# Kernel optimization log

Measured on AMD Instinct MI355X. Metric: run time of the kernel, lower is better.

Reference implementation:

```python
import jax, jax.numpy as jnp
import numpy as np
from jax import lax

SR = 4096.0        # sample_rate_Hz
N_LAYERS = 4
N_STATE = 64       # state_dim
E = 2              # d_inner (expand=2, d_model=1)
K = 4              # depthwise conv kernel
DT_RANK = 1
B, L = 32, 4096


def setup_inputs() -> dict:
    key = jax.random.key(0)
    ks = jax.random.split(key, 10)
    s = 0.02
    x = jax.random.normal(ks[0], (B, L), dtype=jnp.float32)
    W_in   = jax.random.normal(ks[1], (N_LAYERS, 1, 2 * E), jnp.float32) * 1.0
    conv_w = jax.random.normal(ks[2], (N_LAYERS, E, K), jnp.float32) * 0.5
    conv_b = jnp.zeros((N_LAYERS, E), jnp.float32)
    W_x    = jax.random.normal(ks[3], (N_LAYERS, E, DT_RANK + 2 * N_STATE), jnp.float32) * s
    W_dt   = jax.random.normal(ks[4], (N_LAYERS, DT_RANK, E), jnp.float32) * s
    b_dt   = jnp.zeros((N_LAYERS, E), jnp.float32)
    # S4D-real style init: A = -exp(A_log), A_log = log(1..N)
    A_log  = jnp.broadcast_to(jnp.log(jnp.arange(1, N_STATE + 1, dtype=jnp.float32)), (N_LAYERS, E, N_STATE)).copy()
    D_skip = jnp.ones((N_LAYERS, E), jnp.float32)
    W_out  = jax.random.normal(ks[5], (N_LAYERS, E, 1), jnp.float32) * s
    return {"x": x, "W_in": W_in, "conv_w": conv_w, "conv_b": conv_b, "W_x": W_x,
            "W_dt": W_dt, "b_dt": b_dt, "A_log": A_log, "D_skip": D_skip, "W_out": W_out}


def _causal_dwconv(u, w, b):
    # u: [B,L,E], w: [E,K] depthwise causal conv
    Klen = w.shape[1]
    up = jnp.pad(u, ((0, 0), (Klen - 1, 0), (0, 0)))
    y = sum(up[:, k:k + u.shape[1], :] * w[None, None, :, k] for k in range(Klen))
    return y + b


def _selective_scan(u, delta, A, Bm, Cm, Dv):
    # u,delta: [B,L,E]; A: [E,N]; Bm,Cm: [B,L,N]; Dv: [E]
    dA = jnp.exp(delta[..., None] * A)                       # [B,L,E,N]
    dBu = delta[..., None] * Bm[:, :, None, :] * u[..., None]  # [B,L,E,N]

    def step(h, inp):
        dA_t, dBu_t, C_t = inp                               # [B,E,N],[B,E,N],[B,N]
        h = dA_t * h + dBu_t
        y = jnp.einsum('ben,bn->be', h, C_t)
        return h, y

    h0 = jnp.zeros((u.shape[0],) + A.shape, dtype=u.dtype)
    _, ys = lax.scan(step, h0, (dA.transpose(1, 0, 2, 3), dBu.transpose(1, 0, 2, 3), Cm.transpose(1, 0, 2)))
    return ys.transpose(1, 0, 2) + u * Dv                    # [B,L,E]


def _mamba_block(x, W_in, conv_w, conv_b, W_x, W_dt, b_dt, A_log, D_skip, W_out):
    # x: [B,L,1]
    xz = x @ W_in                                            # [B,L,2E]
    u, z = xz[..., :E], xz[..., E:]
    u = jax.nn.silu(_causal_dwconv(u, conv_w, conv_b))       # [B,L,E]
    proj = u @ W_x                                           # [B,L,DT_RANK+2N]
    dt = proj[..., :DT_RANK]
    Bm = proj[..., DT_RANK:DT_RANK + N_STATE]
    Cm = proj[..., DT_RANK + N_STATE:]
    delta = jax.nn.softplus(dt @ W_dt + b_dt) / SR           # [B,L,E], timestep tied to sample rate
    A = -jnp.exp(A_log)                                      # [E,N]
    y = _selective_scan(u, delta, A, Bm, Cm, D_skip)
    y = y * jax.nn.silu(z)
    return y @ W_out + x                                     # residual, [B,L,1]


def reference(x, W_in, conv_w, conv_b, W_x, W_dt, b_dt, A_log, D_skip, W_out):
    h = x[..., None]                                         # [B,L,1]
    for i in range(N_LAYERS):
        h = _mamba_block(h, W_in[i], conv_w[i], conv_b[i], W_x[i], W_dt[i],
                         b_dt[i], A_log[i], D_skip[i], W_out[i])
    return h[..., 0]
```

## Files before the change

kernel.cpp:

```cpp
#include <hip/hip_runtime.h>
#include <hip/hip_bf16.h>


constexpr int   Bsz = 32;
constexpr int   Lsz = 4096;
constexpr int   NC  = 32;
constexpr int   CL  = 128;
constexpr float SRinv = 1.0f / 4096.0f;

__device__ __forceinline__ float sigmoidf_(float v) {
    return 1.0f / (1.0f + __expf(-v));
}

__global__ __launch_bounds__(128) void k_chunk_scan(
    const float* __restrict__ xin,
    const float* __restrict__ W_in,
    const float* __restrict__ conv_w,
    const float* __restrict__ conv_b,
    const float* __restrict__ W_x,
    const float* __restrict__ W_dt,
    const float* __restrict__ b_dt,
    const float* __restrict__ A_log,
    float4* __restrict__ ud,
    float*  __restrict__ Pc,
    float*  __restrict__ Sc)
{
    const int c = blockIdx.x, b = blockIdx.y, tid = threadIdx.x;
    __shared__ float  xs[CL + 3];
    __shared__ float4 s_ud[CL];
    const int base = b * Lsz + c * CL;

    for (int i = tid; i < CL + 3; i += 128) {
        int l = c * CL + i - 3;
        xs[i] = (l >= 0) ? xin[b * Lsz + l] : 0.0f;
    }
    __syncthreads();

    {
        const int t = tid;
        float x0 = xs[t], x1 = xs[t + 1], x2 = xs[t + 2], x3 = xs[t + 3];
        float u[2];
        #pragma unroll
        for (int e = 0; e < 2; e++) {
            float v = W_in[e] * (x0 * conv_w[e * 4 + 0] + x1 * conv_w[e * 4 + 1] +
                                 x2 * conv_w[e * 4 + 2] + x3 * conv_w[e * 4 + 3]) +
                      conv_b[e];
            u[e] = v * sigmoidf_(v);
        }
        float dt = u[0] * W_x[0] + u[1] * W_x[129];
        float dl[2];
        #pragma unroll
        for (int e = 0; e < 2; e++) {
            float a = dt * W_dt[e] + b_dt[e];
            float sp = (a > 20.0f) ? a : log1pf(__expf(a));
            dl[e] = sp * SRinv;
        }
        float4 v4 = make_float4(u[0], u[1], dl[0], dl[1]);
        s_ud[t] = v4;
        ud[base + t] = v4;
    }
    __syncthreads();

    const int e = tid >> 6, n = tid & 63;
    const float Aen = -__expf(A_log[e * 64 + n]);
    const float wb0 = W_x[1 + n], wb1 = W_x[129 + 1 + n];
    float P = 1.0f, S = 0.0f;
    #pragma unroll 8
    for (int l = 0; l < CL; l++) {
        float4 v = s_ud[l];
        float ue = e ? v.y : v.x;
        float d  = e ? v.w : v.z;
        float Bn = v.x * wb0 + v.y * wb1;
        float dA = __expf(d * Aen);
        S = dA * S + (d * ue) * Bn;
        P *= dA;
    }
    const int idx = (b * NC + c) * 128 + tid;
    Pc[idx] = P;
    Sc[idx] = S;
}

__global__ __launch_bounds__(256) void k_combine(
    const float* __restrict__ Pc, const float* __restrict__ Sc,
    float* __restrict__ Hinit)
{
    const int idx = blockIdx.x * 256 + threadIdx.x;
    const int b = idx >> 7, en = idx & 127;
    float h = 0.0f;
    #pragma unroll
    for (int c = 0; c < NC; c++) {
        int o = (b * NC + c) * 128 + en;
        Hinit[o] = h;
        h = Pc[o] * h + Sc[o];
    }
}

__global__ __launch_bounds__(128) void k_output(
    const float* __restrict__ xin,
    const float4* __restrict__ ud,
    const float* __restrict__ Hinit,
    const float* __restrict__ W_in,
    const float* __restrict__ W_x,
    const float* __restrict__ A_log,
    const float* __restrict__ D_skip,
    const float* __restrict__ W_out,
    float* __restrict__ out)
{
    const int c = blockIdx.x, b = blockIdx.y, tid = threadIdx.x;
    constexpr int T = 64;
    __shared__ float4 s_ud[CL];
    __shared__ float  xs[CL];
    __shared__ float  ps[128 * 65];
    __shared__ float  ys[T * 2];
    const int base = b * Lsz + c * CL;

    s_ud[tid] = ud[base + tid];
    xs[tid]   = xin[base + tid];

    const int e = tid >> 6, n = tid & 63;
    const float Aen = -__expf(A_log[e * 64 + n]);
    const float wb0 = W_x[1 + n],  wb1 = W_x[129 + 1 + n];
    const float wc0 = W_x[65 + n], wc1 = W_x[129 + 65 + n];
    float h = Hinit[(b * NC + c) * 128 + tid];
    const float wz0 = W_in[2], wz1 = W_in[3];
    const float D0 = D_skip[0], D1 = D_skip[1];
    const float wo0 = W_out[0], wo1 = W_out[1];
    __syncthreads();

    for (int tile = 0; tile < CL / T; tile++) {
        #pragma unroll 8
        for (int t = 0; t < T; t++) {
            float4 v = s_ud[tile * T + t];
            float ue = e ? v.y : v.x;
            float d  = e ? v.w : v.z;
            float Bn = v.x * wb0 + v.y * wb1;
            float Cn = v.x * wc0 + v.y * wc1;
            float dA = __expf(d * Aen);
            h = dA * h + (d * ue) * Bn;
            ps[(t * 2 + e) * 65 + n] = h * Cn;
        }
        __syncthreads();
        {
            const int r = tid, t = r >> 1, re = r & 1;
            const float* row = &ps[r * 65];
            float a0 = 0, a1 = 0, a2 = 0, a3 = 0;
            #pragma unroll
            for (int j = 0; j < 64; j += 4) {
                a0 += row[j]; a1 += row[j + 1]; a2 += row[j + 2]; a3 += row[j + 3];
            }
            float4 v = s_ud[tile * T + t];
            float ue = re ? v.y : v.x;
            ys[r] = (a0 + a1) + (a2 + a3) + ue * (re ? D1 : D0);
        }
        __syncthreads();
        if (tid < T) {
            int l = tile * T + tid;
            float y0 = ys[tid * 2], y1 = ys[tid * 2 + 1];
            float xv = xs[l];
            float z0 = xv * wz0, z1 = xv * wz1;
            out[base + l] = y0 * (z0 * sigmoidf_(z0)) * wo0 +
                            y1 * (z1 * sigmoidf_(z1)) * wo1 + xv;
        }
        __syncthreads();
    }
}

extern "C" void kernel_launch(void* const* d_in, const int* in_sizes, int n_in,
                              void* d_out, int out_size, void* d_ws, size_t ws_size,
                              hipStream_t stream) {
    const float* x      = (const float*)d_in[0];
    const float* W_in   = (const float*)d_in[1];
    const float* conv_w = (const float*)d_in[2];
    const float* conv_b = (const float*)d_in[3];
    const float* W_x    = (const float*)d_in[4];
    const float* W_dt   = (const float*)d_in[5];
    const float* b_dt   = (const float*)d_in[6];
    const float* A_log  = (const float*)d_in[7];
    const float* D_skip = (const float*)d_in[8];
    const float* W_out  = (const float*)d_in[9];
    float* out = (float*)d_out;

    float* ws   = (float*)d_ws;
    float4* ud  = (float4*)ws;
    float* Pc   = ws + (size_t)Bsz * Lsz * 4;
    float* Sc   = Pc + (size_t)Bsz * NC * 128;
    float* Hi   = Sc + (size_t)Bsz * NC * 128;
    float* buf0 = Hi + (size_t)Bsz * NC * 128;
    float* buf1 = buf0 + (size_t)Bsz * Lsz;

    const float* cur = x;
    for (int i = 0; i < 4; i++) {
        float* o = (i == 3) ? out : ((i & 1) ? buf1 : buf0);
        k_chunk_scan<<<dim3(NC, Bsz), 128, 0, stream>>>(
            cur, W_in + i * 4, conv_w + i * 8, conv_b + i * 2,
            W_x + i * 258, W_dt + i * 2, b_dt + i * 2, A_log + i * 128,
            ud, Pc, Sc);
        k_combine<<<16, 256, 0, stream>>>(Pc, Sc, Hi);
        k_output<<<dim3(NC, Bsz), 128, 0, stream>>>(
            cur, ud, Hi, W_in + i * 4, W_x + i * 258,
            A_log + i * 128, D_skip + i * 2, W_out + i * 2, o);
        cur = o;
    }
}
```

Baseline: 167.6 us.

## Fuse all layers into one persistent kernel with inter-block flag synchronization

Replaces the twelve launches (chunk scan, combine, output for each of four layers) with a single kernel. Each block keeps its chunk resident across all layers and gets the chunk-boundary state through decoupled look-back over earlier chunks' P/S values published with release flags. The conv halo for the next layer is passed from the neighbouring chunk through global memory, guarded by another flag. This removes launch gaps and the ud/intermediate-activation round trips, but relies on all 1024 blocks being co-resident (or scheduled in order) to avoid deadlock, and each block now recomputes a serial look-back of up to 31 chunks.

```diff
diff --git a/kernel.cpp b/kernel.cpp
--- a/kernel.cpp
+++ b/kernel.cpp
@@ -1,18 +1,18 @@
 #include <hip/hip_runtime.h>
-#include <hip/hip_bf16.h>
 
 
 constexpr int   Bsz = 32;
 constexpr int   Lsz = 4096;
 constexpr int   NC  = 32;
 constexpr int   CL  = 128;
+constexpr int   NL  = 4;
 constexpr float SRinv = 1.0f / 4096.0f;
 
 __device__ __forceinline__ float sigmoidf_(float v) {
     return 1.0f / (1.0f + __expf(-v));
 }
 
-__global__ __launch_bounds__(128) void k_chunk_scan(
+__global__ __launch_bounds__(128) void k_mamba_fused(
     const float* __restrict__ xin,
     const float* __restrict__ W_in,
     const float* __restrict__ conv_w,
@@ -21,147 +21,173 @@
     const float* __restrict__ W_dt,
     const float* __restrict__ b_dt,
     const float* __restrict__ A_log,
-    float4* __restrict__ ud,
-    float*  __restrict__ Pc,
-    float*  __restrict__ Sc)
+    const float* __restrict__ D_skip,
+    const float* __restrict__ W_out,
+    int*   __restrict__ flags,
+    float* __restrict__ Pc,
+    float* __restrict__ Sc,
+    float* __restrict__ halo,
+    float* __restrict__ out)
 {
     const int c = blockIdx.x, b = blockIdx.y, tid = threadIdx.x;
+    constexpr int T = 64;
     __shared__ float  xs[CL + 3];
     __shared__ float4 s_ud[CL];
+    __shared__ float  ps[128 * 65];
+    __shared__ float  ys[2 * T];
+    __shared__ float  yn[CL];
+
     const int base = b * Lsz + c * CL;
+    const int e = tid >> 6, n = tid & 63;
 
     for (int i = tid; i < CL + 3; i += 128) {
         int l = c * CL + i - 3;
         xs[i] = (l >= 0) ? xin[b * Lsz + l] : 0.0f;
     }
-    __syncthreads();
-
-    {
-        const int t = tid;
-        float x0 = xs[t], x1 = xs[t + 1], x2 = xs[t + 2], x3 = xs[t + 3];
-        float u[2];
-        #pragma unroll
-        for (int e = 0; e < 2; e++) {
-            float v = W_in[e] * (x0 * conv_w[e * 4 + 0] + x1 * conv_w[e * 4 + 1] +
-                                 x2 * conv_w[e * 4 + 2] + x3 * conv_w[e * 4 + 3]) +
-                      conv_b[e];
-            u[e] = v * sigmoidf_(v);
-        }
-        float dt = u[0] * W_x[0] + u[1] * W_x[129];
-        float dl[2];
-        #pragma unroll
-        for (int e = 0; e < 2; e++) {
-            float a = dt * W_dt[e] + b_dt[e];
-            float sp = (a > 20.0f) ? a : log1pf(__expf(a));
-            dl[e] = sp * SRinv;
-        }
-        float4 v4 = make_float4(u[0], u[1], dl[0], dl[1]);
-        s_ud[t] = v4;
-        ud[base + t] = v4;
-    }
-    __syncthreads();
-
-    const int e = tid >> 6, n = tid & 63;
-    const float Aen = -__expf(A_log[e * 64 + n]);
-    const float wb0 = W_x[1 + n], wb1 = W_x[129 + 1 + n];
-    float P = 1.0f, S = 0.0f;
-    #pragma unroll 8
-    for (int l = 0; l < CL; l++) {
-        float4 v = s_ud[l];
-        float ue = e ? v.y : v.x;
-        float d  = e ? v.w : v.z;
-        float Bn = v.x * wb0 + v.y * wb1;
-        float dA = __expf(d * Aen);
-        S = dA * S + (d * ue) * Bn;
-        P *= dA;
-    }
-    const int idx = (b * NC + c) * 128 + tid;
-    Pc[idx] = P;
-    Sc[idx] = S;
-}
-
-__global__ __launch_bounds__(256) void k_combine(
-    const float* __restrict__ Pc, const float* __restrict__ Sc,
-    float* __restrict__ Hinit)
-{
-    const int idx = blockIdx.x * 256 + threadIdx.x;
-    const int b = idx >> 7, en = idx & 127;
-    float h = 0.0f;
-    #pragma unroll
-    for (int c = 0; c < NC; c++) {
-        int o = (b * NC + c) * 128 + en;
-        Hinit[o] = h;
-        h = Pc[o] * h + Sc[o];
-    }
-}
-
-__global__ __launch_bounds__(128) void k_output(
-    const float* __restrict__ xin,
-    const float4* __restrict__ ud,
-    const float* __restrict__ Hinit,
-    const float* __restrict__ W_in,
-    const float* __restrict__ W_x,
-    const float* __restrict__ A_log,
-    const float* __restrict__ D_skip,
-    const float* __restrict__ W_out,
-    float* __restrict__ out)
-{
-    const int c = blockIdx.x, b = blockIdx.y, tid = threadIdx.x;
-    constexpr int T = 64;
-    __shared__ float4 s_ud[CL];
-    __shared__ float  xs[CL];
-    __shared__ float  ps[128 * 65];
-    __shared__ float  ys[T * 2];
-    const int base = b * Lsz + c * CL;
-
-    s_ud[tid] = ud[base + tid];
-    xs[tid]   = xin[base + tid];
-
-    const int e = tid >> 6, n = tid & 63;
-    const float Aen = -__expf(A_log[e * 64 + n]);
-    const float wb0 = W_x[1 + n],  wb1 = W_x[129 + 1 + n];
-    const float wc0 = W_x[65 + n], wc1 = W_x[129 + 65 + n];
-    float h = Hinit[(b * NC + c) * 128 + tid];
-    const float wz0 = W_in[2], wz1 = W_in[3];
-    const float D0 = D_skip[0], D1 = D_skip[1];
-    const float wo0 = W_out[0], wo1 = W_out[1];
-    __syncthreads();
-
-    for (int tile = 0; tile < CL / T; tile++) {
+
+    for (int layer = 0; layer < NL; ++layer) {
+        const float* Wi = W_in   + layer * 4;
+        const float* cw = conv_w + layer * 8;
+        const float* cb = conv_b + layer * 2;
+        const float* Wx = W_x    + layer * 258;
+        const float* Wd = W_dt   + layer * 2;
+        const float* bd = b_dt   + layer * 2;
+        const float* Al = A_log  + layer * 128;
+        const float* Ds = D_skip + layer * 2;
+        const float* Wo = W_out  + layer * 2;
+        float* Pl = Pc + (size_t)(layer * Bsz + b) * NC * 128;
+        float* Sl = Sc + (size_t)(layer * Bsz + b) * NC * 128;
+        float* Hl = halo + (size_t)(layer * Bsz + b) * NC * 4;
+        int* fA = flags + (layer * Bsz + b) * NC;
+        int* fH = flags + NL * Bsz * NC + (layer * Bsz + b) * NC;
+
+        __syncthreads();
+
+        {
+            const int t = tid;
+            float x0 = xs[t], x1 = xs[t + 1], x2 = xs[t + 2], x3 = xs[t + 3];
+            float u[2];
+            #pragma unroll
+            for (int ee = 0; ee < 2; ee++) {
+                float v = Wi[ee] * (x0 * cw[ee * 4 + 0] + x1 * cw[ee * 4 + 1] +
+                                    x2 * cw[ee * 4 + 2] + x3 * cw[ee * 4 + 3]) +
+                          cb[ee];
+                u[ee] = v * sigmoidf_(v);
+            }
+            float dt = u[0] * Wx[0] + u[1] * Wx[129];
+            float dl[2];
+            #pragma unroll
+            for (int ee = 0; ee < 2; ee++) {
+                float a = dt * Wd[ee] + bd[ee];
+                float sp = (a > 20.0f) ? a : log1pf(__expf(a));
+                dl[ee] = sp * SRinv;
+            }
+            s_ud[t] = make_float4(u[0], u[1], dl[0], dl[1]);
+        }
+        __syncthreads();
+
+        const float Aen = -__expf(Al[e * 64 + n]);
+        const float wb0 = Wx[1 + n], wb1 = Wx[129 + 1 + n];
+        float P = 1.0f, S = 0.0f;
         #pragma unroll 8
-        for (int t = 0; t < T; t++) {
-            float4 v = s_ud[tile * T + t];
+        for (int l = 0; l < CL; l++) {
+            float4 v = s_ud[l];
             float ue = e ? v.y : v.x;
             float d  = e ? v.w : v.z;
             float Bn = v.x * wb0 + v.y * wb1;
-            float Cn = v.x * wc0 + v.y * wc1;
             float dA = __expf(d * Aen);
-            h = dA * h + (d * ue) * Bn;
-            ps[(t * 2 + e) * 65 + n] = h * Cn;
-        }
+            S = dA * S + (d * ue) * Bn;
+            P *= dA;
+        }
+        Pl[c * 128 + tid] = P;
+        Sl[c * 128 + tid] = S;
+        __threadfence();
         __syncthreads();
-        {
-            const int r = tid, t = r >> 1, re = r & 1;
-            const float* row = &ps[r * 65];
-            float a0 = 0, a1 = 0, a2 = 0, a3 = 0;
-            #pragma unroll
-            for (int j = 0; j < 64; j += 4) {
-                a0 += row[j]; a1 += row[j + 1]; a2 += row[j + 2]; a3 += row[j + 3];
-            }
-            float4 v = s_ud[tile * T + t];
-            float ue = re ? v.y : v.x;
-            ys[r] = (a0 + a1) + (a2 + a3) + ue * (re ? D1 : D0);
-        }
-        __syncthreads();
-        if (tid < T) {
-            int l = tile * T + tid;
-            float y0 = ys[tid * 2], y1 = ys[tid * 2 + 1];
-            float xv = xs[l];
-            float z0 = xv * wz0, z1 = xv * wz1;
-            out[base + l] = y0 * (z0 * sigmoidf_(z0)) * wo0 +
-                            y1 * (z1 * sigmoidf_(z1)) * wo1 + xv;
-        }
-        __syncthreads();
+        if (tid == 0)
+            __hip_atomic_store(&fA[c], 1, __ATOMIC_RELEASE, __HIP_MEMORY_SCOPE_AGENT);
+
+        float hin = 0.0f;
+        if (c > 0) {
+            for (int j = tid; j < c; j += 128)
+                while (__hip_atomic_load(&fA[j], __ATOMIC_RELAXED, __HIP_MEMORY_SCOPE_AGENT) == 0)
+                    __builtin_amdgcn_s_sleep(2);
+            __syncthreads();
+            __threadfence();
+            float runS = 0.0f, runP = 1.0f;
+            #pragma unroll 4
+            for (int j = c - 1; j >= 0; --j) {
+                float Sj = Sl[j * 128 + tid];
+                float Pj = Pl[j * 128 + tid];
+                runS = __fmaf_rn(runP, Sj, runS);
+                runP *= Pj;
+            }
+            hin = runS;
+        }
+
+        const float wc0 = Wx[65 + n], wc1 = Wx[129 + 65 + n];
+        const float wz0 = Wi[2], wz1 = Wi[3];
+        const float D0 = Ds[0], D1 = Ds[1];
+        const float wo0 = Wo[0], wo1 = Wo[1];
+        float h = hin;
+        for (int tile = 0; tile < CL / T; ++tile) {
+            #pragma unroll 8
+            for (int t = 0; t < T; t++) {
+                float4 v = s_ud[tile * T + t];
+                float ue = e ? v.y : v.x;
+                float d  = e ? v.w : v.z;
+                float Bn = v.x * wb0 + v.y * wb1;
+                float Cn = v.x * wc0 + v.y * wc1;
+                float dA = __expf(d * Aen);
+                h = dA * h + (d * ue) * Bn;
+                ps[(t * 2 + e) * 65 + n] = h * Cn;
+            }
+            __syncthreads();
+            {
+                const int r = tid, t = r >> 1, re = r & 1;
+                const float* row = &ps[r * 65];
+                float a0 = 0, a1 = 0, a2 = 0, a3 = 0;
+                #pragma unroll
+                for (int j = 0; j < 64; j += 4) {
+                    a0 += row[j]; a1 += row[j + 1]; a2 += row[j + 2]; a3 += row[j + 3];
+                }
+                float4 v = s_ud[tile * T + t];
+                float ue = re ? v.y : v.x;
+                ys[r] = (a0 + a1) + (a2 + a3) + ue * (re ? D1 : D0);
+            }
+            __syncthreads();
+            if (tid < T) {
+                int l = tile * T + tid;
+                float y0 = ys[tid * 2], y1 = ys[tid * 2 + 1];
+                float xv = xs[3 + l];
+                float z0 = xv * wz0, z1 = xv * wz1;
+                float yv = y0 * (z0 * sigmoidf_(z0)) * wo0 +
+                           y1 * (z1 * sigmoidf_(z1)) * wo1 + xv;
+                if (layer == NL - 1) out[base + l] = yv;
+                else                 yn[l] = yv;
+            }
+            __syncthreads();
+        }
+
+        if (layer < NL - 1) {
+            if (tid == 0 && c < NC - 1) {
+                Hl[c * 4 + 0] = yn[125];
+                Hl[c * 4 + 1] = yn[126];
+                Hl[c * 4 + 2] = yn[127];
+                __threadfence();
+                __hip_atomic_store(&fH[c], 1, __ATOMIC_RELEASE, __HIP_MEMORY_SCOPE_AGENT);
+            }
+            xs[3 + tid] = yn[tid];
+            if (tid < 3) {
+                float hv = 0.0f;
+                if (c > 0) {
+                    while (__hip_atomic_load(&fH[c - 1], __ATOMIC_RELAXED, __HIP_MEMORY_SCOPE_AGENT) == 0)
+                        __builtin_amdgcn_s_sleep(2);
+                    __threadfence();
+                    hv = Hl[(c - 1) * 4 + tid];
+                }
+                xs[tid] = hv;
+            }
+        }
     }
 }
 
@@ -180,25 +206,13 @@
     const float* W_out  = (const float*)d_in[9];
     float* out = (float*)d_out;
 
-    float* ws   = (float*)d_ws;
-    float4* ud  = (float4*)ws;
-    float* Pc   = ws + (size_t)Bsz * Lsz * 4;
-    float* Sc   = Pc + (size_t)Bsz * NC * 128;
-    float* Hi   = Sc + (size_t)Bsz * NC * 128;
-    float* buf0 = Hi + (size_t)Bsz * NC * 128;
-    float* buf1 = buf0 + (size_t)Bsz * Lsz;
-
-    const float* cur = x;
-    for (int i = 0; i < 4; i++) {
-        float* o = (i == 3) ? out : ((i & 1) ? buf1 : buf0);
-        k_chunk_scan<<<dim3(NC, Bsz), 128, 0, stream>>>(
-            cur, W_in + i * 4, conv_w + i * 8, conv_b + i * 2,
-            W_x + i * 258, W_dt + i * 2, b_dt + i * 2, A_log + i * 128,
-            ud, Pc, Sc);
-        k_combine<<<16, 256, 0, stream>>>(Pc, Sc, Hi);
-        k_output<<<dim3(NC, Bsz), 128, 0, stream>>>(
-            cur, ud, Hi, W_in + i * 4, W_x + i * 258,
-            A_log + i * 128, D_skip + i * 2, W_out + i * 2, o);
-        cur = o;
-    }
+    int*   flags = (int*)d_ws;
+    float* Pc    = (float*)d_ws + 8192;
+    float* Sc    = Pc + (size_t)NL * Bsz * NC * 128;
+    float* halo  = Sc + (size_t)NL * Bsz * NC * 128;
+
+    hipMemsetAsync(flags, 0, 8192 * sizeof(int), stream);
+    k_mamba_fused<<<dim3(NC, Bsz), 128, 0, stream>>>(
+        x, W_in, conv_w, conv_b, W_x, W_dt, b_dt, A_log, D_skip, W_out,
+        flags, Pc, Sc, halo, out);
 }
```

New measurement: 548.8 us. 3.28x slower.

## Fold chunk-state combine into output kernel and reduce via wave shuffles

Applied to the files above, without the earlier changes.

Removes the separate combine kernel: each output block now recomputes its incoming state by walking the earlier chunks' (P,S) pairs backward. Chunk length drops from 128 to 64, doubling the number of blocks. The per-timestep C·h reduction moves from a padded shared-memory transpose to wave-wide xor shuffles, which drops the large shared buffer and its barriers. In exchange, the prefix recomputation is redundant, costing up to 63 strided global loads per thread, and every timestep now runs six shuffles.

```diff
diff --git a/kernel.cpp b/kernel.cpp
--- a/kernel.cpp
+++ b/kernel.cpp
@@ -1,18 +1,17 @@
 #include <hip/hip_runtime.h>
-#include <hip/hip_bf16.h>
 
 
 constexpr int   Bsz = 32;
 constexpr int   Lsz = 4096;
-constexpr int   NC  = 32;
-constexpr int   CL  = 128;
+constexpr int   NC  = 64;
+constexpr int   CL  = 64;
 constexpr float SRinv = 1.0f / 4096.0f;
 
 __device__ __forceinline__ float sigmoidf_(float v) {
     return 1.0f / (1.0f + __expf(-v));
 }
 
-__global__ __launch_bounds__(128) void k_chunk_scan(
+__global__ __launch_bounds__(128) void k_chunk(
     const float* __restrict__ xin,
     const float* __restrict__ W_in,
     const float* __restrict__ conv_w,
@@ -36,7 +35,7 @@
     }
     __syncthreads();
 
-    {
+    if (tid < CL) {
         const int t = tid;
         float x0 = xs[t], x1 = xs[t + 1], x2 = xs[t + 2], x3 = xs[t + 3];
         float u[2];
@@ -80,25 +79,11 @@
     Sc[idx] = S;
 }
 
-__global__ __launch_bounds__(256) void k_combine(
-    const float* __restrict__ Pc, const float* __restrict__ Sc,
-    float* __restrict__ Hinit)
-{
-    const int idx = blockIdx.x * 256 + threadIdx.x;
-    const int b = idx >> 7, en = idx & 127;
-    float h = 0.0f;
-    #pragma unroll
-    for (int c = 0; c < NC; c++) {
-        int o = (b * NC + c) * 128 + en;
-        Hinit[o] = h;
-        h = Pc[o] * h + Sc[o];
-    }
-}
-
 __global__ __launch_bounds__(128) void k_output(
     const float* __restrict__ xin,
     const float4* __restrict__ ud,
-    const float* __restrict__ Hinit,
+    const float* __restrict__ Pc,
+    const float* __restrict__ Sc,
     const float* __restrict__ W_in,
     const float* __restrict__ W_x,
     const float* __restrict__ A_log,
@@ -107,61 +92,62 @@
     float* __restrict__ out)
 {
     const int c = blockIdx.x, b = blockIdx.y, tid = threadIdx.x;
-    constexpr int T = 64;
     __shared__ float4 s_ud[CL];
-    __shared__ float  xs[CL];
-    __shared__ float  ps[128 * 65];
-    __shared__ float  ys[T * 2];
+    __shared__ float  ys[2 * CL];
     const int base = b * Lsz + c * CL;
 
-    s_ud[tid] = ud[base + tid];
-    xs[tid]   = xin[base + tid];
+    if (tid < CL) s_ud[tid] = ud[base + tid];
 
     const int e = tid >> 6, n = tid & 63;
     const float Aen = -__expf(A_log[e * 64 + n]);
     const float wb0 = W_x[1 + n],  wb1 = W_x[129 + 1 + n];
     const float wc0 = W_x[65 + n], wc1 = W_x[129 + 65 + n];
-    float h = Hinit[(b * NC + c) * 128 + tid];
     const float wz0 = W_in[2], wz1 = W_in[3];
     const float D0 = D_skip[0], D1 = D_skip[1];
     const float wo0 = W_out[0], wo1 = W_out[1];
+
+    float h = 0.0f;
+    if (c > 0) {
+        const float* Pb = Pc + (size_t)b * NC * 128 + tid;
+        const float* Sb = Sc + (size_t)b * NC * 128 + tid;
+        float runS = 0.0f, runP = 1.0f;
+        #pragma unroll 8
+        for (int j = c - 1; j >= 0; --j) {
+            float Sj = Sb[j * 128];
+            float Pj = Pb[j * 128];
+            runS = __fmaf_rn(runP, Sj, runS);
+            runP *= Pj;
+        }
+        h = runS;
+    }
     __syncthreads();
 
-    for (int tile = 0; tile < CL / T; tile++) {
-        #pragma unroll 8
-        for (int t = 0; t < T; t++) {
-            float4 v = s_ud[tile * T + t];
-            float ue = e ? v.y : v.x;
-            float d  = e ? v.w : v.z;
-            float Bn = v.x * wb0 + v.y * wb1;
-            float Cn = v.x * wc0 + v.y * wc1;
-            float dA = __expf(d * Aen);
-            h = dA * h + (d * ue) * Bn;
-            ps[(t * 2 + e) * 65 + n] = h * Cn;
-        }
-        __syncthreads();
-        {
-            const int r = tid, t = r >> 1, re = r & 1;
-            const float* row = &ps[r * 65];
-            float a0 = 0, a1 = 0, a2 = 0, a3 = 0;
-            #pragma unroll
-            for (int j = 0; j < 64; j += 4) {
-                a0 += row[j]; a1 += row[j + 1]; a2 += row[j + 2]; a3 += row[j + 3];
-            }
-            float4 v = s_ud[tile * T + t];
-            float ue = re ? v.y : v.x;
-            ys[r] = (a0 + a1) + (a2 + a3) + ue * (re ? D1 : D0);
-        }
-        __syncthreads();
-        if (tid < T) {
-            int l = tile * T + tid;
-            float y0 = ys[tid * 2], y1 = ys[tid * 2 + 1];
-            float xv = xs[l];
-            float z0 = xv * wz0, z1 = xv * wz1;
-            out[base + l] = y0 * (z0 * sigmoidf_(z0)) * wo0 +
-                            y1 * (z1 * sigmoidf_(z1)) * wo1 + xv;
-        }
-        __syncthreads();
+    #pragma unroll 4
+    for (int t = 0; t < CL; t++) {
+        float4 v = s_ud[t];
+        float ue = e ? v.y : v.x;
+        float d  = e ? v.w : v.z;
+        float Bn = v.x * wb0 + v.y * wb1;
+        float Cn = v.x * wc0 + v.y * wc1;
+        float dA = __expf(d * Aen);
+        h = dA * h + (d * ue) * Bn;
+        float p = h * Cn;
+        p += __shfl_xor(p, 32, 64);
+        p += __shfl_xor(p, 16, 64);
+        p += __shfl_xor(p,  8, 64);
+        p += __shfl_xor(p,  4, 64);
+        p += __shfl_xor(p,  2, 64);
+        p += __shfl_xor(p,  1, 64);
+        if (n == 0) ys[t * 2 + e] = p + (e ? v.y * D1 : v.x * D0);
+    }
+    __syncthreads();
+
+    if (tid < CL) {
+        float y0 = ys[tid * 2], y1 = ys[tid * 2 + 1];
+        float xv = xin[base + tid];
+        float z0 = xv * wz0, z1 = xv * wz1;
+        out[base + tid] = y0 * (z0 * sigmoidf_(z0)) * wo0 +
+                          y1 * (z1 * sigmoidf_(z1)) * wo1 + xv;
     }
 }
 
@@ -184,20 +170,18 @@
     float4* ud  = (float4*)ws;
     float* Pc   = ws + (size_t)Bsz * Lsz * 4;
     float* Sc   = Pc + (size_t)Bsz * NC * 128;
-    float* Hi   = Sc + (size_t)Bsz * NC * 128;
-    float* buf0 = Hi + (size_t)Bsz * NC * 128;
+    float* buf0 = Sc + (size_t)Bsz * NC * 128;
     float* buf1 = buf0 + (size_t)Bsz * Lsz;
 
     const float* cur = x;
     for (int i = 0; i < 4; i++) {
         float* o = (i == 3) ? out : ((i & 1) ? buf1 : buf0);
-        k_chunk_scan<<<dim3(NC, Bsz), 128, 0, stream>>>(
+        k_chunk<<<dim3(NC, Bsz), 128, 0, stream>>>(
             cur, W_in + i * 4, conv_w + i * 8, conv_b + i * 2,
             W_x + i * 258, W_dt + i * 2, b_dt + i * 2, A_log + i * 128,
             ud, Pc, Sc);
-        k_combine<<<16, 256, 0, stream>>>(Pc, Sc, Hi);
         k_output<<<dim3(NC, Bsz), 128, 0, stream>>>(
-            cur, ud, Hi, W_in + i * 4, W_x + i * 258,
+            cur, ud, Pc, Sc, W_in + i * 4, W_x + i * 258,
             A_log + i * 128, D_skip + i * 2, W_out + i * 2, o);
         cur = o;
     }
```

Result: slower. 221.9 us (+32.5%).

## Fold chunk-state combine into output kernel, dropping the combine launch

Applied to the files above, without the earlier changes.

Removes the separate k_combine kernel. Each output block now computes its own initial state by walking the previous chunks' (P,S) pairs in reverse. This saves one kernel launch per layer (four in total) and the Hinit round trip through global memory. In exchange, the later chunks do redundant serial work of up to 31 steps, with two global loads per step.

```diff
diff --git a/kernel.cpp b/kernel.cpp
--- a/kernel.cpp
+++ b/kernel.cpp
@@ -80,25 +80,11 @@
     Sc[idx] = S;
 }
 
-__global__ __launch_bounds__(256) void k_combine(
-    const float* __restrict__ Pc, const float* __restrict__ Sc,
-    float* __restrict__ Hinit)
-{
-    const int idx = blockIdx.x * 256 + threadIdx.x;
-    const int b = idx >> 7, en = idx & 127;
-    float h = 0.0f;
-    #pragma unroll
-    for (int c = 0; c < NC; c++) {
-        int o = (b * NC + c) * 128 + en;
-        Hinit[o] = h;
-        h = Pc[o] * h + Sc[o];
-    }
-}
-
 __global__ __launch_bounds__(128) void k_output(
     const float* __restrict__ xin,
     const float4* __restrict__ ud,
-    const float* __restrict__ Hinit,
+    const float* __restrict__ Pc,
+    const float* __restrict__ Sc,
     const float* __restrict__ W_in,
     const float* __restrict__ W_x,
     const float* __restrict__ A_log,
@@ -121,10 +107,24 @@
     const float Aen = -__expf(A_log[e * 64 + n]);
     const float wb0 = W_x[1 + n],  wb1 = W_x[129 + 1 + n];
     const float wc0 = W_x[65 + n], wc1 = W_x[129 + 65 + n];
-    float h = Hinit[(b * NC + c) * 128 + tid];
     const float wz0 = W_in[2], wz1 = W_in[3];
     const float D0 = D_skip[0], D1 = D_skip[1];
     const float wo0 = W_out[0], wo1 = W_out[1];
+
+    float h = 0.0f;
+    if (c > 0) {
+        const float* Pb = Pc + (size_t)b * NC * 128 + tid;
+        const float* Sb = Sc + (size_t)b * NC * 128 + tid;
+        float runS = 0.0f, runP = 1.0f;
+        #pragma unroll 8
+        for (int j = c - 1; j >= 0; --j) {
+            float Sj = Sb[j * 128];
+            float Pj = Pb[j * 128];
+            runS = __fmaf_rn(runP, Sj, runS);
+            runP *= Pj;
+        }
+        h = runS;
+    }
     __syncthreads();
 
     for (int tile = 0; tile < CL / T; tile++) {
@@ -184,8 +184,7 @@
     float4* ud  = (float4*)ws;
     float* Pc   = ws + (size_t)Bsz * Lsz * 4;
     float* Sc   = Pc + (size_t)Bsz * NC * 128;
-    float* Hi   = Sc + (size_t)Bsz * NC * 128;
-    float* buf0 = Hi + (size_t)Bsz * NC * 128;
+    float* buf0 = Sc + (size_t)Bsz * NC * 128;
     float* buf1 = buf0 + (size_t)Bsz * Lsz;
 
     const float* cur = x;
@@ -195,9 +194,8 @@
             cur, W_in + i * 4, conv_w + i * 8, conv_b + i * 2,
             W_x + i * 258, W_dt + i * 2, b_dt + i * 2, A_log + i * 128,
             ud, Pc, Sc);
-        k_combine<<<16, 256, 0, stream>>>(Pc, Sc, Hi);
         k_output<<<dim3(NC, Bsz), 128, 0, stream>>>(
-            cur, ud, Hi, W_in + i * 4, W_x + i * 258,
+            cur, ud, Pc, Sc, W_in + i * 4, W_x + i * 258,
             A_log + i * 128, D_skip + i * 2, W_out + i * 2, o);
         cur = o;
     }
```

After: 165.7 us. About the same (-1.1%).
